# Kernel optimization log

Measured on AMD Instinct MI355X. Metric: run time of the kernel, lower is better.

Reference implementation:

```python
import jax, jax.numpy as jnp
import numpy as np

B, H, W, C, G = 4, 56, 56, 256, 16
K = 9  # 3x3 deformable kernel
GC = C // G


def _ln(x, g, b, eps=1e-5):
    mu = jnp.mean(x, axis=-1, keepdims=True)
    var = jnp.mean(jnp.square(x - mu), axis=-1, keepdims=True)
    return (x - mu) * jax.lax.rsqrt(var + eps) * g + b


def _gelu(x):
    return jax.nn.gelu(x, approximate=False)  # torch nn.GELU default = exact erf


def _dcnv3_core(x, offset, mask):
    # x: [B,H,W,C]; offset: [B,H,W,G*K*2] (x,y per point); mask: [B,H,W,G,K] softmaxed over K
    xg = x.reshape(B, H * W, G, GC)
    off = offset.reshape(B, H, W, G, K, 2)
    dy, dx = jnp.meshgrid(jnp.arange(-1.0, 2.0), jnp.arange(-1.0, 2.0), indexing="ij")
    dx = dx.reshape(K).astype(x.dtype)
    dy = dy.reshape(K).astype(x.dtype)
    gx = jnp.arange(W, dtype=x.dtype)[None, None, :, None, None]
    gy = jnp.arange(H, dtype=x.dtype)[None, :, None, None, None]
    # sampling locations in unpadded pixel coords (zeros outside image == F.pad + zero grid_sample)
    px = gx + dx + off[..., 0]  # [B,H,W,G,K]
    py = gy + dy + off[..., 1]

    def flat(p):  # [B,H,W,G,K] -> [B, H*W*K, G]
        return p.transpose(0, 1, 2, 4, 3).reshape(B, H * W * K, G)

    pxf, pyf = flat(px), flat(py)
    x0 = jnp.floor(pxf)
    y0 = jnp.floor(pyf)
    acc = jnp.zeros((B, H * W * K, G, GC), x.dtype)
    for cx, cy in ((x0, y0), (x0 + 1, y0), (x0, y0 + 1), (x0 + 1, y0 + 1)):
        wgt = (1 - jnp.abs(pxf - cx)) * (1 - jnp.abs(pyf - cy))
        valid = ((cx >= 0) & (cx < W) & (cy >= 0) & (cy < H)).astype(x.dtype)
        idx = (jnp.clip(cy, 0, H - 1).astype(jnp.int32) * W
               + jnp.clip(cx, 0, W - 1).astype(jnp.int32))[..., None]  # [B,HWK,G,1]
        v = jnp.take_along_axis(xg, idx, axis=1)  # [B,HWK,G,GC]
        acc = acc + (wgt * valid)[..., None] * v
    mf = flat(mask)[..., None]  # [B,HWK,G,1]
    out = (acc * mf).reshape(B, H * W, K, G, GC).sum(axis=2)
    return out.reshape(B, H, W, C)


def _dcn(x, w_in, b_in, w_dw, b_dw, ln_dw_g, ln_dw_b, w_off, b_off,
         w_mask, b_mask, w_out, b_out):
    xp = x @ w_in + b_in  # input projection (value branch)
    x1 = jax.lax.conv_general_dilated(
        x, w_dw, window_strides=(1, 1), padding="SAME",
        dimension_numbers=("NHWC", "HWIO", "NHWC"), feature_group_count=C) + b_dw
    x1 = _gelu(_ln(x1, ln_dw_g, ln_dw_b))  # dw_conv -> LN -> GELU
    offset = x1 @ w_off + b_off  # [B,H,W,G*K*2]
    mask = jax.nn.softmax((x1 @ w_mask + b_mask).reshape(B, H, W, G, K), axis=-1)
    y = _dcnv3_core(xp, offset, mask)
    return y @ w_out + b_out


def _block(x, w_in, b_in, w_dw, b_dw, ln_dw_g, ln_dw_b, w_off, b_off,
           w_mask, b_mask, w_out, b_out, ln1_g, ln1_b,
           w_fc1, b_fc1, w_fc2, b_fc2, ln2_g, ln2_b, gamma1, gamma2):
    # post_norm=True: x = x + gamma1*LN1(dcn(x)); x = x + gamma2*LN2(mlp(x))
    y = _dcn(x, w_in, b_in, w_dw, b_dw, ln_dw_g, ln_dw_b, w_off, b_off,
             w_mask, b_mask, w_out, b_out)
    x = x + gamma1 * _ln(y, ln1_g, ln1_b)
    m = _gelu(x @ w_fc1 + b_fc1) @ w_fc2 + b_fc2  # MLP (dropout = identity)
    x = x + gamma2 * _ln(m, ln2_g, ln2_b)
    return x


def setup_inputs() -> dict:
    key = jax.random.key(0)
    ks = jax.random.split(key, 9)
    f = jnp.float32

    def rn(k, shape, s=0.02):
        return jax.random.normal(k, shape, dtype=f) * s

    return {
        "x": jax.random.normal(ks[0], (B, H, W, C), dtype=f),
        "w_in": rn(ks[1], (C, C)), "b_in": jnp.zeros((C,), f),
        "w_dw": rn(ks[2], (3, 3, 1, C), 0.1), "b_dw": jnp.zeros((C,), f),
        "ln_dw_g": jnp.ones((C,), f), "ln_dw_b": jnp.zeros((C,), f),
        "w_off": rn(ks[3], (C, G * K * 2)), "b_off": jnp.zeros((G * K * 2,), f),
        "w_mask": rn(ks[4], (C, G * K)), "b_mask": jnp.zeros((G * K,), f),
        "w_out": rn(ks[5], (C, C)), "b_out": jnp.zeros((C,), f),
        "ln1_g": jnp.ones((C,), f), "ln1_b": jnp.zeros((C,), f),
        "w_fc1": rn(ks[6], (C, C)), "b_fc1": jnp.zeros((C,), f),
        "w_fc2": rn(ks[7], (C, C)), "b_fc2": jnp.zeros((C,), f),
        "ln2_g": jnp.ones((C,), f), "ln2_b": jnp.zeros((C,), f),
        "gamma1": jnp.ones((C,), f), "gamma2": jnp.ones((C,), f),
    }


def reference(x, w_in, b_in, w_dw, b_dw, ln_dw_g, ln_dw_b, w_off, b_off,
              w_mask, b_mask, w_out, b_out, ln1_g, ln1_b,
              w_fc1, b_fc1, w_fc2, b_fc2, ln2_g, ln2_b, gamma1, gamma2):
    return _block(x, w_in, b_in, w_dw, b_dw, ln_dw_g, ln_dw_b, w_off, b_off,
                  w_mask, b_mask, w_out, b_out, ln1_g, ln1_b,
                  w_fc1, b_fc1, w_fc2, b_fc2, ln2_g, ln2_b, gamma1, gamma2)
```

## Files before the change

### kernel.cpp

```cpp
#include <hip/hip_runtime.h>
#include <math.h>

typedef unsigned short u16;
typedef unsigned int u32;
typedef __attribute__((ext_vector_type(8))) short short8;
typedef __attribute__((ext_vector_type(4))) float f32x4;

#define NB 4
#define NH 56
#define NW 56
#define HW2 (NH*NW)
#define NPIX (NB*HW2)

__device__ __forceinline__ u16 f2b(float f) {
  union { float f; u32 u; } a; a.f = f;
  return (u16)((a.u + 0x7FFFu + ((a.u >> 16) & 1u)) >> 16);
}
__device__ __forceinline__ float b2f(u16 v) {
  union { u32 u; float f; } a; a.u = ((u32)v) << 16; return a.f;
}
__device__ __forceinline__ float gelu_exact(float v) {
  return 0.5f * v * (1.0f + erff(v * 0.70710678118654752f));
}
__device__ __forceinline__ int xcd_swz(int bid, int nwg) {
  const int q = nwg >> 3, r = nwg & 7, x = bid & 7, j = bid >> 3;
  return (x < r ? x * (q + 1) : r * (q + 1) + (x - r) * q) + j;
}
__device__ __forceinline__ u32 swz(int r, int b) {
  return (u32)(r * 512 + ((b ^ (r & 7)) << 4));
}

__global__ __launch_bounds__(256) void prep_kernel(
    const float* __restrict__ w_in, const float* __restrict__ w_out,
    const float* __restrict__ w_fc1, const float* __restrict__ w_fc2,
    const float* __restrict__ w_off, const float* __restrict__ w_mask,
    const float* __restrict__ b_off, const float* __restrict__ b_mask,
    const float* __restrict__ x,
    u16* __restrict__ wT, float* __restrict__ bias_cat, u16* __restrict__ x_bf)
{
  const int blk = blockIdx.x, t = threadIdx.x;
  if (blk < 1456) {
    const float* src; int n, N;
    if      (blk < 256)  { src = w_in;   n = blk;        N = 256; }
    else if (blk < 512)  { src = w_out;  n = blk - 256;  N = 256; }
    else if (blk < 768)  { src = w_fc1;  n = blk - 512;  N = 256; }
    else if (blk < 1024) { src = w_fc2;  n = blk - 768;  N = 256; }
    else if (blk < 1312) { src = w_off;  n = blk - 1024; N = 288; }
    else                 { src = w_mask; n = blk - 1312; N = 144; }
    wT[blk * 256 + t] = f2b(src[t * N + n]);
  } else if (blk < 1456 + 3136) {
    const int cid = blk - 1456;
    float4 v = ((const float4*)x)[cid * 256 + t];
    ushort4 o = make_ushort4(f2b(v.x), f2b(v.y), f2b(v.z), f2b(v.w));
    ((ushort4*)x_bf)[cid * 256 + t] = o;
  } else {
    for (int j = t; j < 432; j += 256)
      bias_cat[j] = (j < 288) ? b_off[j] : b_mask[j - 288];
  }
}

__global__ __launch_bounds__(512) void p2_kernel(
    const u16* __restrict__ x_bf, const u16* __restrict__ wT,
    const float* __restrict__ b_in, u16* __restrict__ xp_bf,
    const float* __restrict__ wdw, const float* __restrict__ bdw,
    const float* __restrict__ lng, const float* __restrict__ lnb,
    u16* __restrict__ x1)
{
  __shared__ u16 As[64 * 256];
  const int t = threadIdx.x;
  if (blockIdx.x < 196) {
    const int m0 = blockIdx.x * 64;
    {
      const int r = t >> 3, j0 = (t & 7) * 4;
      const uint4* src = (const uint4*)(x_bf + (size_t)(m0 + r) * 256);
      #pragma unroll
      for (int i = 0; i < 4; ++i)
        *(uint4*)((char*)As + swz(r, j0 + i)) = src[j0 + i];
    }
    __syncthreads();
    const int l = t & 63, w = t >> 6;
    const int wm = w >> 2, wn = w & 3;
    const int lr = l & 15, lk = l >> 4;
    const int ra0 = wm * 32 + lr, ra1 = wm * 32 + 16 + lr;
    f32x4 acc[2][4] = {};
    const u16* Bbase = wT + (size_t)(wn * 64 + lr) * 256 + lk * 8;
    #pragma unroll
    for (int ks = 0; ks < 8; ++ks) {
      short8 a0 = *(const short8*)((char*)As + swz(ra0, ks * 4 + lk));
      short8 a1 = *(const short8*)((char*)As + swz(ra1, ks * 4 + lk));
      #pragma unroll
      for (int ni = 0; ni < 4; ++ni) {
        short8 b = *(const short8*)(Bbase + ni * 16 * 256 + ks * 32);
        acc[0][ni] = __builtin_amdgcn_mfma_f32_16x16x32_bf16(a0, b, acc[0][ni], 0, 0, 0);
        acc[1][ni] = __builtin_amdgcn_mfma_f32_16x16x32_bf16(a1, b, acc[1][ni], 0, 0, 0);
      }
    }
    const int colb = wn * 64 + lr;
    #pragma unroll
    for (int mi = 0; mi < 2; ++mi)
      #pragma unroll
      for (int r4 = 0; r4 < 4; ++r4) {
        const int row = m0 + wm * 32 + mi * 16 + lk * 4 + r4;
        #pragma unroll
        for (int ni = 0; ni < 4; ++ni)
          xp_bf[(size_t)row * 256 + colb + ni * 16] = f2b(acc[mi][ni][r4] + b_in[colb + ni * 16]);
      }
  } else {
    const int pb = xcd_swz((int)blockIdx.x - 196, 1568);
    const int p = pb * 8 + (t >> 6);
    const int lane = t & 63, c0 = lane * 4;
    const int bb = p / HW2, hw = p - bb * HW2;
    const int h = hw / NW, w = hw - h * NW;
    float4 bd = *(const float4*)(bdw + c0);
    float a0 = bd.x, a1 = bd.y, a2 = bd.z, a3 = bd.w;
    #pragma unroll
    for (int kh = 0; kh < 3; ++kh) {
      const int hh = h + kh - 1;
      if ((unsigned)hh >= NH) continue;
      #pragma unroll
      for (int kw = 0; kw < 3; ++kw) {
        const int ww = w + kw - 1;
        if ((unsigned)ww >= NW) continue;
        ushort4 v = *(const ushort4*)(x_bf + (size_t)(bb * HW2 + hh * NW + ww) * 256 + c0);
        float4 wv = *(const float4*)(wdw + (kh * 3 + kw) * 256 + c0);
        a0 += b2f(v.x) * wv.x; a1 += b2f(v.y) * wv.y;
        a2 += b2f(v.z) * wv.z; a3 += b2f(v.w) * wv.w;
      }
    }
    float s1 = a0 + a1 + a2 + a3;
    float s2 = a0 * a0 + a1 * a1 + a2 * a2 + a3 * a3;
    #pragma unroll
    for (int d = 1; d < 64; d <<= 1) { s1 += __shfl_xor(s1, d); s2 += __shfl_xor(s2, d); }
    const float mu = s1 * (1.0f / 256.0f);
    const float var = s2 * (1.0f / 256.0f) - mu * mu;
    const float rs = rsqrtf(var + 1e-5f);
    float4 lg4 = *(const float4*)(lng + c0);
    float4 lb4 = *(const float4*)(lnb + c0);
    ushort4 o;
    o.x = f2b(gelu_exact((a0 - mu) * rs * lg4.x + lb4.x));
    o.y = f2b(gelu_exact((a1 - mu) * rs * lg4.y + lb4.y));
    o.z = f2b(gelu_exact((a2 - mu) * rs * lg4.z + lb4.z));
    o.w = f2b(gelu_exact((a3 - mu) * rs * lg4.w + lb4.w));
    *(ushort4*)(x1 + (size_t)p * 256 + c0) = o;
  }
}

__global__ __launch_bounds__(256) void gemm_om(
    const u16* __restrict__ A, const u16* __restrict__ Bt,
    const float* __restrict__ bias, u16* __restrict__ Cb, int Ntot)
{
  __shared__ u16 lds[32768];
  char* As = (char*)lds;
  char* Bs = (char*)(lds + 16384);
  const int nN = (Ntot + 63) >> 6;
  const int sb = xcd_swz(blockIdx.x, gridDim.x);
  const int m0 = (sb / nN) * 64;
  const int n0 = (sb % nN) * 64;
  const int t  = threadIdx.x;
  {
    const int r = t >> 2, c0 = t & 3;
    const u16* Ag = A + (size_t)(m0 + r) * 256;
    const int nrow = n0 + r;
    const u16* Bg = Bt + (size_t)nrow * 256;
    const bool bok = nrow < Ntot;
    #pragma unroll
    for (int i = 0; i < 8; ++i) {
      const int b = c0 + i * 4;
      uint4 av = *(const uint4*)(Ag + b * 8);
      *(uint4*)(As + swz(r, b)) = av;
      uint4 bv = make_uint4(0u, 0u, 0u, 0u);
      if (bok) bv = *(const uint4*)(Bg + b * 8);
      *(uint4*)(Bs + swz(r, b)) = bv;
    }
  }
  __syncthreads();
  const int l = t & 63, w = t >> 6;
  const int wm = (w >> 1) << 5, wn = (w & 1) << 5;
  const int lr = l & 15, lk = l >> 4;
  const int ra0 = wm + lr, ra1 = wm + 16 + lr;
  const int rb0 = wn + lr, rb1 = wn + 16 + lr;
  f32x4 acc00 = {}, acc01 = {}, acc10 = {}, acc11 = {};
  #pragma unroll
  for (int ks = 0; ks < 8; ++ks) {
    const int bb = ks * 4 + lk;
    short8 a0 = *(const short8*)(As + swz(ra0, bb));
    short8 a1 = *(const short8*)(As + swz(ra1, bb));
    short8 b0 = *(const short8*)(Bs + swz(rb0, bb));
    short8 b1 = *(const short8*)(Bs + swz(rb1, bb));
    acc00 = __builtin_amdgcn_mfma_f32_16x16x32_bf16(a0, b0, acc00, 0, 0, 0);
    acc01 = __builtin_amdgcn_mfma_f32_16x16x32_bf16(a0, b1, acc01, 0, 0, 0);
    acc10 = __builtin_amdgcn_mfma_f32_16x16x32_bf16(a1, b0, acc10, 0, 0, 0);
    acc11 = __builtin_amdgcn_mfma_f32_16x16x32_bf16(a1, b1, acc11, 0, 0, 0);
  }
  const f32x4 accs[2][2] = {{acc00, acc01}, {acc10, acc11}};
  #pragma unroll
  for (int mi = 0; mi < 2; ++mi)
    #pragma unroll
    for (int ni = 0; ni < 2; ++ni) {
      const int col = n0 + wn + ni * 16 + lr;
      if (col < Ntot) {
        const float bv = bias[col];
        #pragma unroll
        for (int r4 = 0; r4 < 4; ++r4) {
          const int row = m0 + wm + mi * 16 + lk * 4 + r4;
          Cb[(size_t)row * Ntot + col] = f2b(accs[mi][ni][r4] + bv);
        }
      }
    }
}

__global__ __launch_bounds__(256) void dcnv3_kernel(
    const u16* __restrict__ xp, const u16* __restrict__ omb,
    u16* __restrict__ y)
{
  const int sb = xcd_swz(blockIdx.x, NPIX * 32 / 256);
  const int idx = sb * 256 + threadIdx.x;
  const int p = idx >> 5, gh = idx & 31;
  const int g = gh >> 1, hf = gh & 1;
  const int bb = p / HW2, hw = p - bb * HW2;
  const int h = hw / NW, w = hw - h * NW;
  const u16* off = omb + (size_t)p * 432 + g * 18;
  const u16* mk  = omb + (size_t)p * 432 + 288 + g * 9;
  float lg[9];
  float mx = -1e30f;
  #pragma unroll
  for (int k = 0; k < 9; ++k) { lg[k] = b2f(mk[k]); mx = fmaxf(mx, lg[k]); }
  float se = 0.0f;
  #pragma unroll
  for (int k = 0; k < 9; ++k) { lg[k] = __expf(lg[k] - mx); se += lg[k]; }
  const float inv = 1.0f / se;

  float a[8] = {0.f,0.f,0.f,0.f,0.f,0.f,0.f,0.f};
  const u16* base = xp + ((size_t)bb * HW2) * 256 + g * 16 + hf * 8;
  #pragma unroll
  for (int k = 0; k < 9; ++k) {
    const float px = (float)(w + (k % 3) - 1) + b2f(off[2 * k]);
    const float py = (float)(h + (k / 3) - 1) + b2f(off[2 * k + 1]);
    const float fx = floorf(px), fy = floorf(py);
    const int ix = (int)fx, iy = (int)fy;
    const float ax = px - fx, ay = py - fy;
    const float mwt = lg[k] * inv;
    const float w00 = (1.0f - ax) * (1.0f - ay) * mwt;
    const float w10 = ax * (1.0f - ay) * mwt;
    const float w01 = (1.0f - ax) * ay * mwt;
    const float w11 = ax * ay * mwt;
    auto corner = [&](int cx, int cy, float wt) {
      if (cx < 0 || cx >= NW || cy < 0 || cy >= NH) return;
      short8 v = *(const short8*)(base + (size_t)(cy * NW + cx) * 256);
      #pragma unroll
      for (int j = 0; j < 8; ++j) a[j] += wt * b2f((u16)v[j]);
    };
    corner(ix,     iy,     w00);
    corner(ix + 1, iy,     w10);
    corner(ix,     iy + 1, w01);
    corner(ix + 1, iy + 1, w11);
  }
  u16 tmp[8];
  #pragma unroll
  for (int j = 0; j < 8; ++j) tmp[j] = f2b(a[j]);
  *(uint4*)(y + ((size_t)p * 256 + g * 16 + hf * 8)) = *(const uint4*)(tmp);
}

__global__ __launch_bounds__(512) void mega3_kernel(
    const u16* __restrict__ ybf, const u16* __restrict__ wT,
    const float* __restrict__ x, const float* __restrict__ b_out,
    const float* __restrict__ gamma1, const float* __restrict__ ln1g,
    const float* __restrict__ ln1b, const float* __restrict__ b_fc1,
    const float* __restrict__ b_fc2, const float* __restrict__ gamma2,
    const float* __restrict__ ln2g, const float* __restrict__ ln2b,
    float* __restrict__ out)
{
  __shared__ u16 As[64 * 256];
  __shared__ float redS[64][4], redQ[64][4];
  const int t = threadIdx.x;
  const int m0 = blockIdx.x * 64;
  const int l = t & 63, w = t >> 6;
  const int wm = w >> 2, wn = w & 3;
  const int lr = l & 15, lk = l >> 4;
  const int ra0 = wm * 32 + lr, ra1 = wm * 32 + 16 + lr;
  const int colb = wn * 64 + lr;

  {
    const int r = t >> 3, j0 = (t & 7) * 4;
    const uint4* src = (const uint4*)(ybf + (size_t)(m0 + r) * 256);
    #pragma unroll
    for (int i = 0; i < 4; ++i)
      *(uint4*)((char*)As + swz(r, j0 + i)) = src[j0 + i];
  }
  __syncthreads();

  f32x4 acc[2][4];
  auto do_gemm = [&](const u16* Bt) {
    #pragma unroll
    for (int mi = 0; mi < 2; ++mi)
      #pragma unroll
      for (int ni = 0; ni < 4; ++ni) acc[mi][ni] = (f32x4){0.f,0.f,0.f,0.f};
    const u16* Bbase = Bt + (size_t)(wn * 64 + lr) * 256 + lk * 8;
    #pragma unroll
    for (int ks = 0; ks < 8; ++ks) {
      short8 a0 = *(const short8*)((char*)As + swz(ra0, ks * 4 + lk));
      short8 a1 = *(const short8*)((char*)As + swz(ra1, ks * 4 + lk));
      #pragma unroll
      for (int ni = 0; ni < 4; ++ni) {
        short8 b = *(const short8*)(Bbase + ni * 16 * 256 + ks * 32);
        acc[0][ni] = __builtin_amdgcn_mfma_f32_16x16x32_bf16(a0, b, acc[0][ni], 0, 0, 0);
        acc[1][ni] = __builtin_amdgcn_mfma_f32_16x16x32_bf16(a1, b, acc[1][ni], 0, 0, 0);
      }
    }
  };
  auto lds_write_b16 = [&](int row, int col, u16 v) {
    *(u16*)((char*)As + row * 512 + (((col >> 3) ^ (row & 7)) << 4) + (col & 7) * 2) = v;
  };
  auto ln_reduce = [&](const float bv[4], float s1[2][4], float s2[2][4]) {
    #pragma unroll
    for (int mi = 0; mi < 2; ++mi)
      #pragma unroll
      for (int r4 = 0; r4 < 4; ++r4) {
        float s = 0.f, q = 0.f;
        #pragma unroll
        for (int ni = 0; ni < 4; ++ni) {
          const float v = acc[mi][ni][r4] + bv[ni];
          s += v; q += v * v;
        }
        s1[mi][r4] = s; s2[mi][r4] = q;
      }
    #pragma unroll
    for (int d = 1; d < 16; d <<= 1)
      #pragma unroll
      for (int mi = 0; mi < 2; ++mi)
        #pragma unroll
        for (int r4 = 0; r4 < 4; ++r4) {
          s1[mi][r4] += __shfl_xor(s1[mi][r4], d);
          s2[mi][r4] += __shfl_xor(s2[mi][r4], d);
        }
    if (lr == 0) {
      #pragma unroll
      for (int mi = 0; mi < 2; ++mi)
        #pragma unroll
        for (int r4 = 0; r4 < 4; ++r4) {
          const int rl = wm * 32 + mi * 16 + lk * 4 + r4;
          redS[rl][wn] = s1[mi][r4];
          redQ[rl][wn] = s2[mi][r4];
        }
    }
    __syncthreads();
  };

  do_gemm(wT + 256 * 256);
  float bv1[4], s1[2][4], s2[2][4];
  #pragma unroll
  for (int ni = 0; ni < 4; ++ni) bv1[ni] = b_out[colb + ni * 16];
  ln_reduce(bv1, s1, s2);

  float x2r[2][4][4];
  {
    float gmv[4], lgv[4], lbv[4];
    #pragma unroll
    for (int ni = 0; ni < 4; ++ni) {
      gmv[ni] = gamma1[colb + ni * 16];
      lgv[ni] = ln1g[colb + ni * 16];
      lbv[ni] = ln1b[colb + ni * 16];
    }
    #pragma unroll
    for (int mi = 0; mi < 2; ++mi)
      #pragma unroll
      for (int r4 = 0; r4 < 4; ++r4) {
        const int rl = wm * 32 + mi * 16 + lk * 4 + r4;
        const float S = redS[rl][0] + redS[rl][1] + redS[rl][2] + redS[rl][3];
        const float Q = redQ[rl][0] + redQ[rl][1] + redQ[rl][2] + redQ[rl][3];
        const float mu = S * (1.0f / 256.0f);
        const float var = Q * (1.0f / 256.0f) - mu * mu;
        const float rs = rsqrtf(var + 1e-5f);
        const int row = m0 + rl;
        #pragma unroll
        for (int ni = 0; ni < 4; ++ni) {
          const float v = acc[mi][ni][r4] + bv1[ni];
          const float o = x[(size_t)row * 256 + colb + ni * 16]
                        + gmv[ni] * ((v - mu) * rs * lgv[ni] + lbv[ni]);
          x2r[mi][r4][ni] = o;
          lds_write_b16(rl, colb + ni * 16, f2b(o));
        }
      }
  }
  __syncthreads();

  do_gemm(wT + 512 * 256);
  float m1v[2][4][4];
  #pragma unroll
  for (int mi = 0; mi < 2; ++mi)
    #pragma unroll
    for (int r4 = 0; r4 < 4; ++r4)
      #pragma unroll
      for (int ni = 0; ni < 4; ++ni)
        m1v[mi][r4][ni] = gelu_exact(acc[mi][ni][r4] + b_fc1[colb + ni * 16]);
  __syncthreads();
  #pragma unroll
  for (int mi = 0; mi < 2; ++mi)
    #pragma unroll
    for (int r4 = 0; r4 < 4; ++r4) {
      const int rl = wm * 32 + mi * 16 + lk * 4 + r4;
      #pragma unroll
      for (int ni = 0; ni < 4; ++ni)
        lds_write_b16(rl, colb + ni * 16, f2b(m1v[mi][r4][ni]));
    }
  __syncthreads();

  do_gemm(wT + 768 * 256);
  float bv3[4];
  #pragma unroll
  for (int ni = 0; ni < 4; ++ni) bv3[ni] = b_fc2[colb + ni * 16];
  ln_reduce(bv3, s1, s2);
  {
    float gmv[4], lgv[4], lbv[4];
    #pragma unroll
    for (int ni = 0; ni < 4; ++ni) {
      gmv[ni] = gamma2[colb + ni * 16];
      lgv[ni] = ln2g[colb + ni * 16];
      lbv[ni] = ln2b[colb + ni * 16];
    }
    #pragma unroll
    for (int mi = 0; mi < 2; ++mi)
      #pragma unroll
      for (int r4 = 0; r4 < 4; ++r4) {
        const int rl = wm * 32 + mi * 16 + lk * 4 + r4;
        const float S = redS[rl][0] + redS[rl][1] + redS[rl][2] + redS[rl][3];
        const float Q = redQ[rl][0] + redQ[rl][1] + redQ[rl][2] + redQ[rl][3];
        const float mu = S * (1.0f / 256.0f);
        const float var = Q * (1.0f / 256.0f) - mu * mu;
        const float rs = rsqrtf(var + 1e-5f);
        const int row = m0 + rl;
        #pragma unroll
        for (int ni = 0; ni < 4; ++ni) {
          const float v = acc[mi][ni][r4] + bv3[ni];
          out[(size_t)row * 256 + colb + ni * 16] =
              x2r[mi][r4][ni] + gmv[ni] * ((v - mu) * rs * lgv[ni] + lbv[ni]);
        }
      }
  }
}

static constexpr size_t OFF_WT  = 0;
static constexpr size_t OFF_BC  = 745472;
static constexpr size_t OFF_XBF = 747520;
static constexpr size_t OFF_XP  = 7170048;
static constexpr size_t OFF_X1  = 13592576;
static constexpr size_t OFF_OMB = 20015104;
static constexpr size_t OFF_Y   = 30853120;

extern "C" void kernel_launch(void* const* d_in, const int* in_sizes, int n_in,
                              void* d_out, int out_size, void* d_ws, size_t ws_size,
                              hipStream_t stream)
{
  const float* x      = (const float*)d_in[0];
  const float* w_in   = (const float*)d_in[1];
  const float* b_in   = (const float*)d_in[2];
  const float* w_dw   = (const float*)d_in[3];
  const float* b_dw   = (const float*)d_in[4];
  const float* ln_dw_g= (const float*)d_in[5];
  const float* ln_dw_b= (const float*)d_in[6];
  const float* w_off  = (const float*)d_in[7];
  const float* b_off  = (const float*)d_in[8];
  const float* w_mask = (const float*)d_in[9];
  const float* b_mask = (const float*)d_in[10];
  const float* w_out  = (const float*)d_in[11];
  const float* b_out  = (const float*)d_in[12];
  const float* ln1_g  = (const float*)d_in[13];
  const float* ln1_b  = (const float*)d_in[14];
  const float* w_fc1  = (const float*)d_in[15];
  const float* b_fc1  = (const float*)d_in[16];
  const float* w_fc2  = (const float*)d_in[17];
  const float* b_fc2  = (const float*)d_in[18];
  const float* ln2_g  = (const float*)d_in[19];
  const float* ln2_b  = (const float*)d_in[20];
  const float* gamma1 = (const float*)d_in[21];
  const float* gamma2 = (const float*)d_in[22];
  float* out = (float*)d_out;

  char* ws = (char*)d_ws;
  u16*   wT    = (u16*)  (ws + OFF_WT);
  float* bcat  = (float*)(ws + OFF_BC);
  u16*   x_bf  = (u16*)  (ws + OFF_XBF);
  u16*   xp_bf = (u16*)  (ws + OFF_XP);
  u16*   x1    = (u16*)  (ws + OFF_X1);
  u16*   omb   = (u16*)  (ws + OFF_OMB);
  u16*   ybf   = (u16*)  (ws + OFF_Y);

  prep_kernel<<<dim3(1456 + 3136 + 1), 256, 0, stream>>>(
      w_in, w_out, w_fc1, w_fc2, w_off, w_mask, b_off, b_mask, x, wT, bcat, x_bf);
  p2_kernel<<<dim3(196 + 1568), 512, 0, stream>>>(
      x_bf, wT, b_in, xp_bf, w_dw, b_dw, ln_dw_g, ln_dw_b, x1);
  gemm_om<<<dim3(196 * 7), 256, 0, stream>>>(x1, wT + 1024 * 256, bcat, omb, 432);
  dcnv3_kernel<<<dim3(NPIX * 32 / 256), 256, 0, stream>>>(xp_bf, omb, ybf);
  mega3_kernel<<<dim3(196), 512, 0, stream>>>(
      ybf, wT, x, b_out, gamma1, ln1_g, ln1_b, b_fc1, b_fc2,
      gamma2, ln2_g, ln2_b, out);
}
```

Before: 105.6 us.

## Fuse depthwise conv+LN+GELU with offset/mask GEMM via LDS tile

The depthwise 3x3 conv, LayerNorm and GELU branch now writes a 64-row tile into shared memory and immediately runs the offset/mask projection GEMM (432 columns) from that tile inside p2_kernel. This removes the x1 intermediate's global round trip and the separate gemm_om launch. In exchange, the fused blocks drop from 1568 to 196, which lowers parallelism and raises per-block register pressure from the 2x7 accumulators. The bilinear corner loads in the dcnv3 kernel also unpack bf16 pairs with shifts and masks instead of per-element conversion.

```diff
diff --git a/kernel.cpp b/kernel.cpp
--- a/kernel.cpp
+++ b/kernel.cpp
@@ -64,10 +64,13 @@
     const float* __restrict__ b_in, u16* __restrict__ xp_bf,
     const float* __restrict__ wdw, const float* __restrict__ bdw,
     const float* __restrict__ lng, const float* __restrict__ lnb,
-    u16* __restrict__ x1)
+    const float* __restrict__ bcat, u16* __restrict__ omb)
 {
   __shared__ u16 As[64 * 256];
   const int t = threadIdx.x;
+  const int l = t & 63, w = t >> 6;
+  const int lr = l & 15, lk = l >> 4;
+
   if (blockIdx.x < 196) {
     const int m0 = blockIdx.x * 64;
     {
@@ -78,9 +81,7 @@
         *(uint4*)((char*)As + swz(r, j0 + i)) = src[j0 + i];
     }
     __syncthreads();
-    const int l = t & 63, w = t >> 6;
     const int wm = w >> 2, wn = w & 3;
-    const int lr = l & 15, lk = l >> 4;
     const int ra0 = wm * 32 + lr, ra1 = wm * 32 + 16 + lr;
     f32x4 acc[2][4] = {};
     const u16* Bbase = wT + (size_t)(wn * 64 + lr) * 256 + lk * 8;
@@ -106,107 +107,88 @@
           xp_bf[(size_t)row * 256 + colb + ni * 16] = f2b(acc[mi][ni][r4] + b_in[colb + ni * 16]);
       }
   } else {
-    const int pb = xcd_swz((int)blockIdx.x - 196, 1568);
-    const int p = pb * 8 + (t >> 6);
-    const int lane = t & 63, c0 = lane * 4;
-    const int bb = p / HW2, hw = p - bb * HW2;
-    const int h = hw / NW, w = hw - h * NW;
-    float4 bd = *(const float4*)(bdw + c0);
-    float a0 = bd.x, a1 = bd.y, a2 = bd.z, a3 = bd.w;
-    #pragma unroll
-    for (int kh = 0; kh < 3; ++kh) {
-      const int hh = h + kh - 1;
-      if ((unsigned)hh >= NH) continue;
-      #pragma unroll
-      for (int kw = 0; kw < 3; ++kw) {
-        const int ww = w + kw - 1;
-        if ((unsigned)ww >= NW) continue;
-        ushort4 v = *(const ushort4*)(x_bf + (size_t)(bb * HW2 + hh * NW + ww) * 256 + c0);
-        float4 wv = *(const float4*)(wdw + (kh * 3 + kw) * 256 + c0);
-        a0 += b2f(v.x) * wv.x; a1 += b2f(v.y) * wv.y;
-        a2 += b2f(v.z) * wv.z; a3 += b2f(v.w) * wv.w;
-      }
-    }
-    float s1 = a0 + a1 + a2 + a3;
-    float s2 = a0 * a0 + a1 * a1 + a2 * a2 + a3 * a3;
-    #pragma unroll
-    for (int d = 1; d < 64; d <<= 1) { s1 += __shfl_xor(s1, d); s2 += __shfl_xor(s2, d); }
-    const float mu = s1 * (1.0f / 256.0f);
-    const float var = s2 * (1.0f / 256.0f) - mu * mu;
-    const float rs = rsqrtf(var + 1e-5f);
-    float4 lg4 = *(const float4*)(lng + c0);
-    float4 lb4 = *(const float4*)(lnb + c0);
-    ushort4 o;
-    o.x = f2b(gelu_exact((a0 - mu) * rs * lg4.x + lb4.x));
-    o.y = f2b(gelu_exact((a1 - mu) * rs * lg4.y + lb4.y));
-    o.z = f2b(gelu_exact((a2 - mu) * rs * lg4.z + lb4.z));
-    o.w = f2b(gelu_exact((a3 - mu) * rs * lg4.w + lb4.w));
-    *(ushort4*)(x1 + (size_t)p * 256 + c0) = o;
-  }
-}
-
-__global__ __launch_bounds__(256) void gemm_om(
-    const u16* __restrict__ A, const u16* __restrict__ Bt,
-    const float* __restrict__ bias, u16* __restrict__ Cb, int Ntot)
-{
-  __shared__ u16 lds[32768];
-  char* As = (char*)lds;
-  char* Bs = (char*)(lds + 16384);
-  const int nN = (Ntot + 63) >> 6;
-  const int sb = xcd_swz(blockIdx.x, gridDim.x);
-  const int m0 = (sb / nN) * 64;
-  const int n0 = (sb % nN) * 64;
-  const int t  = threadIdx.x;
-  {
-    const int r = t >> 2, c0 = t & 3;
-    const u16* Ag = A + (size_t)(m0 + r) * 256;
-    const int nrow = n0 + r;
-    const u16* Bg = Bt + (size_t)nrow * 256;
-    const bool bok = nrow < Ntot;
-    #pragma unroll
-    for (int i = 0; i < 8; ++i) {
-      const int b = c0 + i * 4;
-      uint4 av = *(const uint4*)(Ag + b * 8);
-      *(uint4*)(As + swz(r, b)) = av;
-      uint4 bv = make_uint4(0u, 0u, 0u, 0u);
-      if (bok) bv = *(const uint4*)(Bg + b * 8);
-      *(uint4*)(Bs + swz(r, b)) = bv;
-    }
-  }
-  __syncthreads();
-  const int l = t & 63, w = t >> 6;
-  const int wm = (w >> 1) << 5, wn = (w & 1) << 5;
-  const int lr = l & 15, lk = l >> 4;
-  const int ra0 = wm + lr, ra1 = wm + 16 + lr;
-  const int rb0 = wn + lr, rb1 = wn + 16 + lr;
-  f32x4 acc00 = {}, acc01 = {}, acc10 = {}, acc11 = {};
-  #pragma unroll
-  for (int ks = 0; ks < 8; ++ks) {
-    const int bb = ks * 4 + lk;
-    short8 a0 = *(const short8*)(As + swz(ra0, bb));
-    short8 a1 = *(const short8*)(As + swz(ra1, bb));
-    short8 b0 = *(const short8*)(Bs + swz(rb0, bb));
-    short8 b1 = *(const short8*)(Bs + swz(rb1, bb));
-    acc00 = __builtin_amdgcn_mfma_f32_16x16x32_bf16(a0, b0, acc00, 0, 0, 0);
-    acc01 = __builtin_amdgcn_mfma_f32_16x16x32_bf16(a0, b1, acc01, 0, 0, 0);
-    acc10 = __builtin_amdgcn_mfma_f32_16x16x32_bf16(a1, b0, acc10, 0, 0, 0);
-    acc11 = __builtin_amdgcn_mfma_f32_16x16x32_bf16(a1, b1, acc11, 0, 0, 0);
-  }
-  const f32x4 accs[2][2] = {{acc00, acc01}, {acc10, acc11}};
-  #pragma unroll
-  for (int mi = 0; mi < 2; ++mi)
-    #pragma unroll
-    for (int ni = 0; ni < 2; ++ni) {
-      const int col = n0 + wn + ni * 16 + lr;
-      if (col < Ntot) {
-        const float bv = bias[col];
-        #pragma unroll
-        for (int r4 = 0; r4 < 4; ++r4) {
-          const int row = m0 + wm + mi * 16 + lk * 4 + r4;
-          Cb[(size_t)row * Ntot + col] = f2b(accs[mi][ni][r4] + bv);
-        }
-      }
-    }
+    const int pb = xcd_swz((int)blockIdx.x - 196, 196);
+    const int m0 = pb * 64;
+    const int c0 = l * 4;
+    const float4 bd  = *(const float4*)(bdw + c0);
+    const float4 lg4 = *(const float4*)(lng + c0);
+    const float4 lb4 = *(const float4*)(lnb + c0);
+    float4 wv9[9];
+    #pragma unroll
+    for (int k = 0; k < 9; ++k) wv9[k] = *(const float4*)(wdw + k * 256 + c0);
+
+    #pragma unroll
+    for (int it = 0; it < 8; ++it) {
+      const int pl = it * 8 + w;
+      const int p = m0 + pl;
+      const int bb = p / HW2, hw = p - bb * HW2;
+      const int h = hw / NW, wx = hw - h * NW;
+      float a0 = bd.x, a1 = bd.y, a2 = bd.z, a3 = bd.w;
+      #pragma unroll
+      for (int kh = 0; kh < 3; ++kh) {
+        const int hh = h + kh - 1;
+        if ((unsigned)hh >= NH) continue;
+        #pragma unroll
+        for (int kw = 0; kw < 3; ++kw) {
+          const int ww = wx + kw - 1;
+          if ((unsigned)ww >= NW) continue;
+          ushort4 v = *(const ushort4*)(x_bf + (size_t)(bb * HW2 + hh * NW + ww) * 256 + c0);
+          const float4 wv = wv9[kh * 3 + kw];
+          a0 += b2f(v.x) * wv.x; a1 += b2f(v.y) * wv.y;
+          a2 += b2f(v.z) * wv.z; a3 += b2f(v.w) * wv.w;
+        }
+      }
+      float s1 = a0 + a1 + a2 + a3;
+      float s2 = a0 * a0 + a1 * a1 + a2 * a2 + a3 * a3;
+      #pragma unroll
+      for (int d = 1; d < 64; d <<= 1) { s1 += __shfl_xor(s1, d); s2 += __shfl_xor(s2, d); }
+      const float mu = s1 * (1.0f / 256.0f);
+      const float var = s2 * (1.0f / 256.0f) - mu * mu;
+      const float rs = rsqrtf(var + 1e-5f);
+      const u16 o0 = f2b(gelu_exact((a0 - mu) * rs * lg4.x + lb4.x));
+      const u16 o1 = f2b(gelu_exact((a1 - mu) * rs * lg4.y + lb4.y));
+      const u16 o2 = f2b(gelu_exact((a2 - mu) * rs * lg4.z + lb4.z));
+      const u16 o3 = f2b(gelu_exact((a3 - mu) * rs * lg4.w + lb4.w));
+      uint2 pk;
+      pk.x = (u32)o0 | ((u32)o1 << 16);
+      pk.y = (u32)o2 | ((u32)o3 << 16);
+      *(uint2*)((char*)As + pl * 512 + (((c0 >> 3) ^ (pl & 7)) << 4) + (c0 & 7) * 2) = pk;
+    }
+    __syncthreads();
+
+    const int wm = w >> 2, wn = w & 3;
+    const int nt = (wn == 3) ? 6 : 7;
+    const int ra0 = wm * 32 + lr, ra1 = wm * 32 + 16 + lr;
+    f32x4 acc[2][7] = {};
+    #pragma unroll
+    for (int ks = 0; ks < 8; ++ks) {
+      short8 a0 = *(const short8*)((char*)As + swz(ra0, ks * 4 + lk));
+      short8 a1 = *(const short8*)((char*)As + swz(ra1, ks * 4 + lk));
+      #pragma unroll
+      for (int ni = 0; ni < 7; ++ni) {
+        if (ni < nt) {
+          const int nrow = 1024 + (wn * 7 + ni) * 16 + lr;
+          short8 b = *(const short8*)(wT + (size_t)nrow * 256 + lk * 8 + ks * 32);
+          acc[0][ni] = __builtin_amdgcn_mfma_f32_16x16x32_bf16(a0, b, acc[0][ni], 0, 0, 0);
+          acc[1][ni] = __builtin_amdgcn_mfma_f32_16x16x32_bf16(a1, b, acc[1][ni], 0, 0, 0);
+        }
+      }
+    }
+    #pragma unroll
+    for (int ni = 0; ni < 7; ++ni) {
+      if (ni < nt) {
+        const int col = (wn * 7 + ni) * 16 + lr;
+        const float bv = bcat[col];
+        #pragma unroll
+        for (int mi = 0; mi < 2; ++mi)
+          #pragma unroll
+          for (int r4 = 0; r4 < 4; ++r4) {
+            const int row = m0 + wm * 32 + mi * 16 + lk * 4 + r4;
+            omb[(size_t)row * 432 + col] = f2b(acc[mi][ni][r4] + bv);
+          }
+      }
+    }
+  }
 }
 
 __global__ __launch_bounds__(256) void dcnv3_kernel(
@@ -246,9 +228,15 @@
     const float w11 = ax * ay * mwt;
     auto corner = [&](int cx, int cy, float wt) {
       if (cx < 0 || cx >= NW || cy < 0 || cy >= NH) return;
-      short8 v = *(const short8*)(base + (size_t)(cy * NW + cx) * 256);
-      #pragma unroll
-      for (int j = 0; j < 8; ++j) a[j] += wt * b2f((u16)v[j]);
+      uint4 v = *(const uint4*)(base + (size_t)(cy * NW + cx) * 256);
+      const u32 wv[4] = {v.x, v.y, v.z, v.w};
+      #pragma unroll
+      for (int j = 0; j < 4; ++j) {
+        union { u32 u; float f; } lo, hi;
+        lo.u = wv[j] << 16; hi.u = wv[j] & 0xffff0000u;
+        a[2 * j]     += wt * lo.f;
+        a[2 * j + 1] += wt * hi.f;
+      }
     };
     corner(ix,     iy,     w00);
     corner(ix + 1, iy,     w10);
@@ -443,9 +431,8 @@
 static constexpr size_t OFF_BC  = 745472;
 static constexpr size_t OFF_XBF = 747520;
 static constexpr size_t OFF_XP  = 7170048;
-static constexpr size_t OFF_X1  = 13592576;
-static constexpr size_t OFF_OMB = 20015104;
-static constexpr size_t OFF_Y   = 30853120;
+static constexpr size_t OFF_OMB = 13592576;
+static constexpr size_t OFF_Y   = 24430592;
 
 extern "C" void kernel_launch(void* const* d_in, const int* in_sizes, int n_in,
                               void* d_out, int out_size, void* d_ws, size_t ws_size,
@@ -481,15 +468,13 @@
   float* bcat  = (float*)(ws + OFF_BC);
   u16*   x_bf  = (u16*)  (ws + OFF_XBF);
   u16*   xp_bf = (u16*)  (ws + OFF_XP);
-  u16*   x1    = (u16*)  (ws + OFF_X1);
   u16*   omb   = (u16*)  (ws + OFF_OMB);
   u16*   ybf   = (u16*)  (ws + OFF_Y);
 
   prep_kernel<<<dim3(1456 + 3136 + 1), 256, 0, stream>>>(
       w_in, w_out, w_fc1, w_fc2, w_off, w_mask, b_off, b_mask, x, wT, bcat, x_bf);
-  p2_kernel<<<dim3(196 + 1568), 512, 0, stream>>>(
-      x_bf, wT, b_in, xp_bf, w_dw, b_dw, ln_dw_g, ln_dw_b, x1);
-  gemm_om<<<dim3(196 * 7), 256, 0, stream>>>(x1, wT + 1024 * 256, bcat, omb, 432);
+  p2_kernel<<<dim3(196 + 196), 512, 0, stream>>>(
+      x_bf, wT, b_in, xp_bf, w_dw, b_dw, ln_dw_g, ln_dw_b, bcat, omb);
   dcnv3_kernel<<<dim3(NPIX * 32 / 256), 256, 0, stream>>>(xp_bf, omb, ybf);
   mega3_kernel<<<dim3(196), 512, 0, stream>>>(
       ybf, wT, x, b_out, gamma1, ln1_g, ln1_b, b_fc1, b_fc2,
```

After: 116.8 us. 1.11x slower.

## Drop bf16 staging of x, stage offsets/masks in LDS for DCN sampling

Applied to the files above, without the earlier changes.

Removes the prep pass that converted x to a bf16 copy. The projection GEMM now converts fp32 to bf16 while filling shared memory, and the depthwise conv reads fp32 x directly, saving one full write and read of the activation. The dcnv3 kernel now loads each block's 8 pixel offset/mask rows cooperatively into LDS with vector loads, and unpacks bf16 pairs with bit ops. The trade-off is that the depthwise conv reads twice as many bytes per tap from fp32 x, and dcnv3 gains a barrier.

```diff
diff --git a/kernel.cpp b/kernel.cpp
--- a/kernel.cpp
+++ b/kernel.cpp
@@ -35,8 +35,7 @@
     const float* __restrict__ w_fc1, const float* __restrict__ w_fc2,
     const float* __restrict__ w_off, const float* __restrict__ w_mask,
     const float* __restrict__ b_off, const float* __restrict__ b_mask,
-    const float* __restrict__ x,
-    u16* __restrict__ wT, float* __restrict__ bias_cat, u16* __restrict__ x_bf)
+    u16* __restrict__ wT, float* __restrict__ bias_cat)
 {
   const int blk = blockIdx.x, t = threadIdx.x;
   if (blk < 1456) {
@@ -48,11 +47,6 @@
     else if (blk < 1312) { src = w_off;  n = blk - 1024; N = 288; }
     else                 { src = w_mask; n = blk - 1312; N = 144; }
     wT[blk * 256 + t] = f2b(src[t * N + n]);
-  } else if (blk < 1456 + 3136) {
-    const int cid = blk - 1456;
-    float4 v = ((const float4*)x)[cid * 256 + t];
-    ushort4 o = make_ushort4(f2b(v.x), f2b(v.y), f2b(v.z), f2b(v.w));
-    ((ushort4*)x_bf)[cid * 256 + t] = o;
   } else {
     for (int j = t; j < 432; j += 256)
       bias_cat[j] = (j < 288) ? b_off[j] : b_mask[j - 288];
@@ -60,7 +54,7 @@
 }
 
 __global__ __launch_bounds__(512) void p2_kernel(
-    const u16* __restrict__ x_bf, const u16* __restrict__ wT,
+    const float* __restrict__ xf, const u16* __restrict__ wT,
     const float* __restrict__ b_in, u16* __restrict__ xp_bf,
     const float* __restrict__ wdw, const float* __restrict__ bdw,
     const float* __restrict__ lng, const float* __restrict__ lnb,
@@ -71,11 +65,17 @@
   if (blockIdx.x < 196) {
     const int m0 = blockIdx.x * 64;
     {
-      const int r = t >> 3, j0 = (t & 7) * 4;
-      const uint4* src = (const uint4*)(x_bf + (size_t)(m0 + r) * 256);
-      #pragma unroll
-      for (int i = 0; i < 4; ++i)
-        *(uint4*)((char*)As + swz(r, j0 + i)) = src[j0 + i];
+      const int r = t >> 3;
+      const float4* src = (const float4*)(xf + (size_t)(m0 + r) * 256);
+      #pragma unroll
+      for (int i = 0; i < 8; ++i) {
+        const int f4 = (t & 7) + i * 8;
+        float4 v = src[f4];
+        uint2 pk;
+        pk.x = (u32)f2b(v.x) | ((u32)f2b(v.y) << 16);
+        pk.y = (u32)f2b(v.z) | ((u32)f2b(v.w) << 16);
+        *(uint2*)((char*)As + swz(r, f4 >> 1) + (f4 & 1) * 8) = pk;
+      }
     }
     __syncthreads();
     const int l = t & 63, w = t >> 6;
@@ -121,10 +121,10 @@
       for (int kw = 0; kw < 3; ++kw) {
         const int ww = w + kw - 1;
         if ((unsigned)ww >= NW) continue;
-        ushort4 v = *(const ushort4*)(x_bf + (size_t)(bb * HW2 + hh * NW + ww) * 256 + c0);
+        float4 v = *(const float4*)(xf + (size_t)(bb * HW2 + hh * NW + ww) * 256 + c0);
         float4 wv = *(const float4*)(wdw + (kh * 3 + kw) * 256 + c0);
-        a0 += b2f(v.x) * wv.x; a1 += b2f(v.y) * wv.y;
-        a2 += b2f(v.z) * wv.z; a3 += b2f(v.w) * wv.w;
+        a0 += v.x * wv.x; a1 += v.y * wv.y;
+        a2 += v.z * wv.z; a3 += v.w * wv.w;
       }
     }
     float s1 = a0 + a1 + a2 + a3;
@@ -213,14 +213,23 @@
     const u16* __restrict__ xp, const u16* __restrict__ omb,
     u16* __restrict__ y)
 {
-  const int sb = xcd_swz(blockIdx.x, NPIX * 32 / 256);
-  const int idx = sb * 256 + threadIdx.x;
-  const int p = idx >> 5, gh = idx & 31;
+  __shared__ u16 lom[8 * 432];
+  const int sb = xcd_swz(blockIdx.x, NPIX / 8);
+  const int p0 = sb * 8;
+  for (int i = threadIdx.x; i < 432; i += 256) {
+    const int row = i / 54, u = i - row * 54;
+    *(uint4*)(lom + row * 432 + u * 8) =
+        *(const uint4*)(omb + (size_t)(p0 + row) * 432 + u * 8);
+  }
+  __syncthreads();
+  const int tid = threadIdx.x;
+  const int lp = tid >> 5, gh = tid & 31;
   const int g = gh >> 1, hf = gh & 1;
+  const int p = p0 + lp;
   const int bb = p / HW2, hw = p - bb * HW2;
   const int h = hw / NW, w = hw - h * NW;
-  const u16* off = omb + (size_t)p * 432 + g * 18;
-  const u16* mk  = omb + (size_t)p * 432 + 288 + g * 9;
+  const u16* off = lom + lp * 432 + g * 18;
+  const u16* mk  = lom + lp * 432 + 288 + g * 9;
   float lg[9];
   float mx = -1e30f;
   #pragma unroll
@@ -246,9 +255,15 @@
     const float w11 = ax * ay * mwt;
     auto corner = [&](int cx, int cy, float wt) {
       if (cx < 0 || cx >= NW || cy < 0 || cy >= NH) return;
-      short8 v = *(const short8*)(base + (size_t)(cy * NW + cx) * 256);
-      #pragma unroll
-      for (int j = 0; j < 8; ++j) a[j] += wt * b2f((u16)v[j]);
+      uint4 v = *(const uint4*)(base + (size_t)(cy * NW + cx) * 256);
+      const u32 wv[4] = {v.x, v.y, v.z, v.w};
+      #pragma unroll
+      for (int j = 0; j < 4; ++j) {
+        union { u32 u; float f; } lo, hi;
+        lo.u = wv[j] << 16; hi.u = wv[j] & 0xffff0000u;
+        a[2 * j]     += wt * lo.f;
+        a[2 * j + 1] += wt * hi.f;
+      }
     };
     corner(ix,     iy,     w00);
     corner(ix + 1, iy,     w10);
@@ -441,11 +456,10 @@
 
 static constexpr size_t OFF_WT  = 0;
 static constexpr size_t OFF_BC  = 745472;
-static constexpr size_t OFF_XBF = 747520;
-static constexpr size_t OFF_XP  = 7170048;
-static constexpr size_t OFF_X1  = 13592576;
-static constexpr size_t OFF_OMB = 20015104;
-static constexpr size_t OFF_Y   = 30853120;
+static constexpr size_t OFF_XP  = 747520;
+static constexpr size_t OFF_X1  = 7170048;
+static constexpr size_t OFF_OMB = 13592576;
+static constexpr size_t OFF_Y   = 24430592;
 
 extern "C" void kernel_launch(void* const* d_in, const int* in_sizes, int n_in,
                               void* d_out, int out_size, void* d_ws, size_t ws_size,
@@ -479,18 +493,17 @@
   char* ws = (char*)d_ws;
   u16*   wT    = (u16*)  (ws + OFF_WT);
   float* bcat  = (float*)(ws + OFF_BC);
-  u16*   x_bf  = (u16*)  (ws + OFF_XBF);
   u16*   xp_bf = (u16*)  (ws + OFF_XP);
   u16*   x1    = (u16*)  (ws + OFF_X1);
   u16*   omb   = (u16*)  (ws + OFF_OMB);
   u16*   ybf   = (u16*)  (ws + OFF_Y);
 
-  prep_kernel<<<dim3(1456 + 3136 + 1), 256, 0, stream>>>(
-      w_in, w_out, w_fc1, w_fc2, w_off, w_mask, b_off, b_mask, x, wT, bcat, x_bf);
+  prep_kernel<<<dim3(1457), 256, 0, stream>>>(
+      w_in, w_out, w_fc1, w_fc2, w_off, w_mask, b_off, b_mask, wT, bcat);
   p2_kernel<<<dim3(196 + 1568), 512, 0, stream>>>(
-      x_bf, wT, b_in, xp_bf, w_dw, b_dw, ln_dw_g, ln_dw_b, x1);
+      x, wT, b_in, xp_bf, w_dw, b_dw, ln_dw_g, ln_dw_b, x1);
   gemm_om<<<dim3(196 * 7), 256, 0, stream>>>(x1, wT + 1024 * 256, bcat, omb, 432);
-  dcnv3_kernel<<<dim3(NPIX * 32 / 256), 256, 0, stream>>>(xp_bf, omb, ybf);
+  dcnv3_kernel<<<dim3(NPIX / 8), 256, 0, stream>>>(xp_bf, omb, ybf);
   mega3_kernel<<<dim3(196), 512, 0, stream>>>(
       ybf, wT, x, b_out, gamma1, ln1_g, ln1_b, b_fc1, b_fc2,
       gamma2, ln2_g, ln2_b, out);
```

Measured after the change: 101.1 us. -4.2%, faster.
